# Kernel tuning notes

Hardware: AMD Instinct MI355X
Metric: run time of the kernel (lower is better)

Reference implementation:

```python
import jax, jax.numpy as jnp
import numpy as np

COMMITMENT_COST = 0.25


def setup_inputs() -> dict:
    key = jax.random.key(0)
    k1, k2 = jax.random.split(key)
    z = jax.random.normal(k1, (16, 1024, 256), dtype=jnp.float32)
    embedding = jax.random.normal(k2, (8192, 256), dtype=jnp.float32)
    return {"z": z, "embedding": embedding}


def reference(z, embedding):
    B, N, C = z.shape
    flat = z.reshape(-1, C)  # (B*N, C)
    d = (
        jnp.sum(flat * flat, axis=1, keepdims=True)
        + jnp.sum(embedding * embedding, axis=1)
        - 2.0 * jnp.matmul(flat, embedding.T)
    )  # (B*N, K)
    idx = jnp.argmin(d, axis=1)  # (B*N,)
    quantized = jnp.take(embedding, idx, axis=0).reshape(B, N, C)
    # losses (matching torch detach semantics; in eval fwd-only these are plain MSEs)
    e_latent_loss = jnp.mean((jax.lax.stop_gradient(quantized) - z) ** 2)
    q_latent_loss = jnp.mean((quantized - jax.lax.stop_gradient(z)) ** 2)
    vq_loss = q_latent_loss + COMMITMENT_COST * e_latent_loss
    # straight-through estimator
    quantized_ste = z + jax.lax.stop_gradient(quantized - z)
    encoding_indices = idx.reshape(B, N)
    return quantized_ste, vq_loss, encoding_indices
```

## Files before the change

kernel.cpp:

```cpp
#include <hip/hip_runtime.h>
#include <math.h>

#define MROWS   16384
#define KCODES  8192
#define CDIM    256

#define LOSS_OFF 4194304
#define IDXOFF   4194305

#define NSPLIT  8
#define WS_EF   0
#define WS_ZF   (WS_EF + KCODES * CDIM * 2)
#define WS_EN   (WS_ZF + MROWS * CDIM * 2)
#define WS_PI   (WS_EN + KCODES * 4)
#define WS_PD   (WS_PI + NSPLIT * MROWS * 4)

#define CODES_PER_SPLIT (KCODES / NSPLIT)
#define STEPS32 (CODES_PER_SPLIT / 32)

typedef float    v4f __attribute__((ext_vector_type(4)));
typedef _Float16 v8h __attribute__((ext_vector_type(8)));
typedef __attribute__((address_space(1))) const unsigned int gu32;
typedef __attribute__((address_space(3))) unsigned int su32;

__global__ void conv_kernel(const float* __restrict__ z,
                            const float* __restrict__ emb,
                            char* __restrict__ ws,
                            float* __restrict__ loss_slot) {
    int t = blockIdx.x * 256 + threadIdx.x;
    const int NZ = MROWS * 32;
    const float4* s4;
    _Float16* dst;
    int j, c;
    bool isE = (t >= NZ);
    if (!isE) {
        j = t >> 5; c = t & 31;
        s4 = (const float4*)(z + (size_t)j * CDIM) + c * 2;
        dst = (_Float16*)(ws + WS_ZF);
    } else {
        int u = t - NZ;
        j = u >> 5; c = u & 31;
        s4 = (const float4*)(emb + (size_t)j * CDIM) + c * 2;
        dst = (_Float16*)(ws + WS_EF);
    }
    float4 a = s4[0], b = s4[1];
    v8h h;
    h[0] = (_Float16)a.x; h[1] = (_Float16)a.y;
    h[2] = (_Float16)a.z; h[3] = (_Float16)a.w;
    h[4] = (_Float16)b.x; h[5] = (_Float16)b.y;
    h[6] = (_Float16)b.z; h[7] = (_Float16)b.w;
    *(v8h*)(dst + ((size_t)(j >> 4) * 32 + c) * 128 + (j & 15) * 8) = h;
    if (isE) {
        float s = a.x * a.x + a.y * a.y + a.z * a.z + a.w * a.w +
                  b.x * b.x + b.y * b.y + b.z * b.z + b.w * b.w;
#pragma unroll
        for (int m = 1; m <= 16; m <<= 1) s += __shfl_xor(s, m, 64);
        if (c == 0) ((float*)(ws + WS_EN))[j] = s + 1024.0f;
    }
    if (t == 0) *loss_slot = 0.f;
}

__global__ __launch_bounds__(256, 2)
void vq_pass1_kernel(const char* __restrict__ ws_c, char* __restrict__ ws) {
    __shared__ __attribute__((aligned(16))) char bbuf[2][16384];
    int tid  = threadIdx.x;
    int lane = tid & 63;
    int w    = tid >> 6;
    int tm   = lane & 15;
    int q    = lane >> 4;

    int b  = blockIdx.x;
    int sp = b & 7;
    int rb = b >> 3;
    int r0 = rb * 256 + w * 64;

    const _Float16* zf_g = (const _Float16*)(ws_c + WS_ZF);
    v8h zf[4][8];
#pragma unroll
    for (int mi = 0; mi < 4; ++mi) {
        const _Float16* zr = zf_g + (size_t)((r0 >> 4) + mi) * 4096 + q * 128 + tm * 8;
#pragma unroll
        for (int kc = 0; kc < 8; ++kc)
            zf[mi][kc] = *(const v8h*)(zr + kc * 512);
    }

    const char*  efb  = ws_c + WS_EF + (size_t)(sp * 64) * 8192;
    const float* en_g = (const float*)(ws_c + WS_EN);

#define STAGE(st, bi) do {                                                      \
        const char* g0 = efb + (size_t)(st) * 16384 + w * 4096 + lane * 16;     \
        char* l0 = &bbuf[bi][w * 4096];                                         \
        __builtin_amdgcn_global_load_lds((gu32*)g0, (su32*)l0, 16, 0, 0);       \
        __builtin_amdgcn_global_load_lds((gu32*)(g0 + 1024),                    \
                                         (su32*)(l0 + 1024), 16, 0, 0);         \
        __builtin_amdgcn_global_load_lds((gu32*)(g0 + 2048),                    \
                                         (su32*)(l0 + 2048), 16, 0, 0);         \
        __builtin_amdgcn_global_load_lds((gu32*)(g0 + 3072),                    \
                                         (su32*)(l0 + 3072), 16, 0, 0);         \
    } while (0)

    unsigned rk[16];
#pragma unroll
    for (int s = 0; s < 16; ++s) rk[s] = 0xFFFFFFFFu;

    STAGE(0, 0);
    float enr0 = en_g[sp * 1024 + tm];
    float enr1 = en_g[sp * 1024 + 16 + tm];
    __syncthreads();

#pragma unroll 1
    for (int st = 0; st < STEPS32; ++st) {
        int cur = st & 1;
        if (st < STEPS32 - 1) STAGE(st + 1, cur ^ 1);
        int stn = (st < STEPS32 - 1) ? st + 1 : st;
        float enn0 = en_g[sp * 1024 + stn * 32 + tm];
        float enn1 = en_g[sp * 1024 + stn * 32 + 16 + tm];

#pragma unroll
        for (int ct = 0; ct < 2; ++ct) {
            const char* lb = &bbuf[cur][ct * 8192 + q * 256 + tm * 16];
            v8h bf[8];
#pragma unroll
            for (int kc = 0; kc < 8; ++kc) bf[kc] = *(const v8h*)(lb + kc * 1024);

            v4f acc[4];
#pragma unroll
            for (int mi = 0; mi < 4; ++mi)
                acc[mi] = __builtin_amdgcn_mfma_f32_16x16x32_f16(zf[mi][0], bf[0], (v4f)0.f, 0, 0, 0);
#pragma unroll
            for (int kc = 1; kc < 8; ++kc)
#pragma unroll
                for (int mi = 0; mi < 4; ++mi)
                    acc[mi] = __builtin_amdgcn_mfma_f32_16x16x32_f16(zf[mi][kc], bf[kc], acc[mi], 0, 0, 0);

            float enc = ct ? enr1 : enr0;
            unsigned tag = (unsigned)(st * 2 + ct);
#pragma unroll
            for (int mi = 0; mi < 4; ++mi)
#pragma unroll
                for (int r = 0; r < 4; ++r) {
                    float s = fmaf(-2.f, acc[mi][r], enc);
                    unsigned key = (__float_as_uint(s) << 6) | tag;
                    int slot = mi * 4 + r;
                    rk[slot] = key < rk[slot] ? key : rk[slot];
                }
        }
        enr0 = enn0; enr1 = enn1;
        __syncthreads();
    }
#undef STAGE

#pragma unroll
    for (int slot = 0; slot < 16; ++slot) {
        unsigned k = rk[slot];
        int      t_ = tm;
#pragma unroll
        for (int m = 1; m <= 8; m <<= 1) {
            unsigned k2 = __shfl_xor(k, m, 64);
            int      t2 = __shfl_xor(t_, m, 64);
            if (k2 < k || (k2 == k && t2 < t_)) { k = k2; t_ = t2; }
        }
        if (tm == 0) {
            int row = r0 + (slot >> 2) * 16 + q * 4 + (slot & 3);
            int bi  = sp * 1024 + (int)(k & 63u) * 16 + t_;
            ((int*)(ws + WS_PI))[sp * MROWS + row] = bi;
            ((float*)(ws + WS_PD))[sp * MROWS + row] =
                __uint_as_float((k >> 6) | (17u << 26));
        }
    }
}

__global__ void rerank_out_kernel(const float* __restrict__ z,
                                  const float* __restrict__ emb,
                                  const char* __restrict__ ws,
                                  float* __restrict__ out) {
    __shared__ float wsum[4];
    const int*   pi = (const int*)(ws + WS_PI);
    const float* pd = (const float*)(ws + WS_PD);
    int tid = threadIdx.x, lane = tid & 63, w = tid >> 6;
    int g = lane >> 3, sub = lane & 7;
    const float4* e4 = (const float4*)emb;
    const float4* z4 = (const float4*)z;
    float lsum = 0.f;

#pragma unroll 1
    for (int it = 0; it < 4; ++it) {
        int row = it * 4096 + blockIdx.x * 4 + w;
        int ci   = pi[g * MROWS + row];
        float pg = pd[g * MROWS + row];
        float dmin = pg;
#pragma unroll
        for (int m = 8; m <= 32; m <<= 1) dmin = fminf(dmin, __shfl_xor(dmin, m, 64));
        float s;
        if (pg <= dmin + 0.75f) {
            s = 0.f;
#pragma unroll
            for (int j = 0; j < 8; ++j) {
                float4 ev = e4[(size_t)ci * 64 + sub * 8 + j];
                float4 zv = z4[(size_t)row * 64 + sub * 8 + j];
                float dx = ev.x - zv.x, dy = ev.y - zv.y;
                float dz = ev.z - zv.z, dw = ev.w - zv.w;
                s += dx * dx + dy * dy + dz * dz + dw * dw;
            }
        } else {
            s = 3e38f;
        }
#pragma unroll
        for (int m = 1; m <= 4; m <<= 1) s += __shfl_xor(s, m, 64);
        float dv = s; int di = ci;
#pragma unroll
        for (int m = 8; m <= 32; m <<= 1) {
            float d2 = __shfl_xor(dv, m, 64);
            int   i2 = __shfl_xor(di, m, 64);
            if (d2 < dv || (d2 == dv && i2 < di)) { dv = d2; di = i2; }
        }
        if (lane == 0) out[IDXOFF + row] = (float)di;
        float4 qv = e4[(size_t)di * 64 + lane];
        float4 zv = z4[(size_t)row * 64 + lane];
        float dx = qv.x - zv.x, dy = qv.y - zv.y;
        float dz = qv.z - zv.z, dw = qv.w - zv.w;
        float4 o;
        o.x = zv.x + dx; o.y = zv.y + dy; o.z = zv.z + dz; o.w = zv.w + dw;
        ((float4*)out)[(size_t)row * 64 + lane] = o;
        lsum += dx * dx + dy * dy + dz * dz + dw * dw;
    }

#pragma unroll
    for (int m = 32; m >= 1; m >>= 1) lsum += __shfl_xor(lsum, m, 64);
    if (lane == 0) wsum[w] = lsum;
    __syncthreads();
    if (tid == 0)
        atomicAdd(out + LOSS_OFF,
                  (wsum[0] + wsum[1] + wsum[2] + wsum[3]) * (1.25f / 4194304.f));
}

extern "C" void kernel_launch(void* const* d_in, const int* in_sizes, int n_in,
                              void* d_out, int out_size, void* d_ws, size_t ws_size,
                              hipStream_t stream) {
    const float* z   = (const float*)d_in[0];
    const float* emb = (const float*)d_in[1];
    float* out = (float*)d_out;
    char*  ws  = (char*)d_ws;

    hipLaunchKernelGGL(conv_kernel, dim3((MROWS + KCODES) * 32 / 256), dim3(256),
                       0, stream, z, emb, ws, out + LOSS_OFF);
    hipLaunchKernelGGL(vq_pass1_kernel, dim3((MROWS / 256) * NSPLIT), dim3(256),
                       0, stream, ws, ws);
    hipLaunchKernelGGL(rerank_out_kernel, dim3(1024), dim3(256),
                       0, stream, z, emb, ws, out);
}
```

Baseline: 168.5 us.

## Fuse z fp16 conversion into distance kernel and double code tile per stage

Removes the separate z-to-fp16 conversion pass and its workspace buffer: the distance kernel now loads z in fp32 directly into registers and converts it there, overlapping with the first codebook stage. The LDS double buffer grows to 64 codes per stage, halving the number of barrier-separated iterations, and code norms are now loaded per tile rather than prefetched. This saves a global write and read of z in fp16, but each of the 8 split blocks now rereads fp32 z, and the larger LDS use may reduce occupancy.

Result: slower. 173.6 us (+3.0%).

```diff
diff --git a/kernel.cpp b/kernel.cpp
--- a/kernel.cpp
+++ b/kernel.cpp
@@ -10,59 +10,44 @@
 
 #define NSPLIT  8
 #define WS_EF   0
-#define WS_ZF   (WS_EF + KCODES * CDIM * 2)
-#define WS_EN   (WS_ZF + MROWS * CDIM * 2)
+#define WS_EN   (WS_EF + KCODES * CDIM * 2)
 #define WS_PI   (WS_EN + KCODES * 4)
 #define WS_PD   (WS_PI + NSPLIT * MROWS * 4)
 
 #define CODES_PER_SPLIT (KCODES / NSPLIT)
-#define STEPS32 (CODES_PER_SPLIT / 32)
+#define STEPS64 (CODES_PER_SPLIT / 64)
 
 typedef float    v4f __attribute__((ext_vector_type(4)));
 typedef _Float16 v8h __attribute__((ext_vector_type(8)));
 typedef __attribute__((address_space(1))) const unsigned int gu32;
 typedef __attribute__((address_space(3))) unsigned int su32;
 
-__global__ void conv_kernel(const float* __restrict__ z,
-                            const float* __restrict__ emb,
+__global__ void conv_kernel(const float* __restrict__ emb,
                             char* __restrict__ ws,
                             float* __restrict__ loss_slot) {
     int t = blockIdx.x * 256 + threadIdx.x;
-    const int NZ = MROWS * 32;
-    const float4* s4;
-    _Float16* dst;
-    int j, c;
-    bool isE = (t >= NZ);
-    if (!isE) {
-        j = t >> 5; c = t & 31;
-        s4 = (const float4*)(z + (size_t)j * CDIM) + c * 2;
-        dst = (_Float16*)(ws + WS_ZF);
-    } else {
-        int u = t - NZ;
-        j = u >> 5; c = u & 31;
-        s4 = (const float4*)(emb + (size_t)j * CDIM) + c * 2;
-        dst = (_Float16*)(ws + WS_EF);
-    }
+    int j = t >> 5, c = t & 31;
+    const float4* s4 = (const float4*)(emb + (size_t)j * CDIM) + c * 2;
     float4 a = s4[0], b = s4[1];
     v8h h;
     h[0] = (_Float16)a.x; h[1] = (_Float16)a.y;
     h[2] = (_Float16)a.z; h[3] = (_Float16)a.w;
     h[4] = (_Float16)b.x; h[5] = (_Float16)b.y;
     h[6] = (_Float16)b.z; h[7] = (_Float16)b.w;
-    *(v8h*)(dst + ((size_t)(j >> 4) * 32 + c) * 128 + (j & 15) * 8) = h;
-    if (isE) {
-        float s = a.x * a.x + a.y * a.y + a.z * a.z + a.w * a.w +
-                  b.x * b.x + b.y * b.y + b.z * b.z + b.w * b.w;
-#pragma unroll
-        for (int m = 1; m <= 16; m <<= 1) s += __shfl_xor(s, m, 64);
-        if (c == 0) ((float*)(ws + WS_EN))[j] = s + 1024.0f;
-    }
+    *(v8h*)((_Float16*)(ws + WS_EF) +
+            ((size_t)(j >> 4) * 32 + c) * 128 + (j & 15) * 8) = h;
+    float s = a.x * a.x + a.y * a.y + a.z * a.z + a.w * a.w +
+              b.x * b.x + b.y * b.y + b.z * b.z + b.w * b.w;
+#pragma unroll
+    for (int m = 1; m <= 16; m <<= 1) s += __shfl_xor(s, m, 64);
+    if (c == 0) ((float*)(ws + WS_EN))[j] = s + 1024.0f;
     if (t == 0) *loss_slot = 0.f;
 }
 
 __global__ __launch_bounds__(256, 2)
-void vq_pass1_kernel(const char* __restrict__ ws_c, char* __restrict__ ws) {
-    __shared__ __attribute__((aligned(16))) char bbuf[2][16384];
+void vq_pass1_kernel(const float* __restrict__ z,
+                     const char* __restrict__ ws_c, char* __restrict__ ws) {
+    __shared__ __attribute__((aligned(16))) char bbuf[2][32768];
     int tid  = threadIdx.x;
     int lane = tid & 63;
     int w    = tid >> 6;
@@ -74,22 +59,12 @@
     int rb = b >> 3;
     int r0 = rb * 256 + w * 64;
 
-    const _Float16* zf_g = (const _Float16*)(ws_c + WS_ZF);
-    v8h zf[4][8];
-#pragma unroll
-    for (int mi = 0; mi < 4; ++mi) {
-        const _Float16* zr = zf_g + (size_t)((r0 >> 4) + mi) * 4096 + q * 128 + tm * 8;
-#pragma unroll
-        for (int kc = 0; kc < 8; ++kc)
-            zf[mi][kc] = *(const v8h*)(zr + kc * 512);
-    }
-
     const char*  efb  = ws_c + WS_EF + (size_t)(sp * 64) * 8192;
     const float* en_g = (const float*)(ws_c + WS_EN);
 
 #define STAGE(st, bi) do {                                                      \
-        const char* g0 = efb + (size_t)(st) * 16384 + w * 4096 + lane * 16;     \
-        char* l0 = &bbuf[bi][w * 4096];                                         \
+        const char* g0 = efb + (size_t)(st) * 32768 + w * 8192 + lane * 16;     \
+        char* l0 = &bbuf[bi][w * 8192];                                         \
         __builtin_amdgcn_global_load_lds((gu32*)g0, (su32*)l0, 16, 0, 0);       \
         __builtin_amdgcn_global_load_lds((gu32*)(g0 + 1024),                    \
                                          (su32*)(l0 + 1024), 16, 0, 0);         \
@@ -97,31 +72,53 @@
                                          (su32*)(l0 + 2048), 16, 0, 0);         \
         __builtin_amdgcn_global_load_lds((gu32*)(g0 + 3072),                    \
                                          (su32*)(l0 + 3072), 16, 0, 0);         \
+        __builtin_amdgcn_global_load_lds((gu32*)(g0 + 4096),                    \
+                                         (su32*)(l0 + 4096), 16, 0, 0);         \
+        __builtin_amdgcn_global_load_lds((gu32*)(g0 + 5120),                    \
+                                         (su32*)(l0 + 5120), 16, 0, 0);         \
+        __builtin_amdgcn_global_load_lds((gu32*)(g0 + 6144),                    \
+                                         (su32*)(l0 + 6144), 16, 0, 0);         \
+        __builtin_amdgcn_global_load_lds((gu32*)(g0 + 7168),                    \
+                                         (su32*)(l0 + 7168), 16, 0, 0);         \
     } while (0)
 
+    STAGE(0, 0);
+
+    v8h zf[4][8];
+#pragma unroll
+    for (int mi = 0; mi < 4; ++mi) {
+        const float* zr = z + (size_t)(r0 + mi * 16 + tm) * 256 + q * 8;
+#pragma unroll
+        for (int kc = 0; kc < 8; ++kc) {
+            float4 a = *(const float4*)(zr + kc * 32);
+            float4 bb = *(const float4*)(zr + kc * 32 + 4);
+            v8h h;
+            h[0] = (_Float16)a.x;  h[1] = (_Float16)a.y;
+            h[2] = (_Float16)a.z;  h[3] = (_Float16)a.w;
+            h[4] = (_Float16)bb.x; h[5] = (_Float16)bb.y;
+            h[6] = (_Float16)bb.z; h[7] = (_Float16)bb.w;
+            zf[mi][kc] = h;
+        }
+    }
+
     unsigned rk[16];
 #pragma unroll
     for (int s = 0; s < 16; ++s) rk[s] = 0xFFFFFFFFu;
 
-    STAGE(0, 0);
-    float enr0 = en_g[sp * 1024 + tm];
-    float enr1 = en_g[sp * 1024 + 16 + tm];
     __syncthreads();
 
 #pragma unroll 1
-    for (int st = 0; st < STEPS32; ++st) {
+    for (int st = 0; st < STEPS64; ++st) {
         int cur = st & 1;
-        if (st < STEPS32 - 1) STAGE(st + 1, cur ^ 1);
-        int stn = (st < STEPS32 - 1) ? st + 1 : st;
-        float enn0 = en_g[sp * 1024 + stn * 32 + tm];
-        float enn1 = en_g[sp * 1024 + stn * 32 + 16 + tm];
-
-#pragma unroll
-        for (int ct = 0; ct < 2; ++ct) {
+        if (st < STEPS64 - 1) STAGE(st + 1, cur ^ 1);
+
+#pragma unroll
+        for (int ct = 0; ct < 4; ++ct) {
             const char* lb = &bbuf[cur][ct * 8192 + q * 256 + tm * 16];
             v8h bf[8];
 #pragma unroll
             for (int kc = 0; kc < 8; ++kc) bf[kc] = *(const v8h*)(lb + kc * 1024);
+            float enc = en_g[sp * 1024 + st * 64 + ct * 16 + tm];
 
             v4f acc[4];
 #pragma unroll
@@ -133,8 +130,7 @@
                 for (int mi = 0; mi < 4; ++mi)
                     acc[mi] = __builtin_amdgcn_mfma_f32_16x16x32_f16(zf[mi][kc], bf[kc], acc[mi], 0, 0, 0);
 
-            float enc = ct ? enr1 : enr0;
-            unsigned tag = (unsigned)(st * 2 + ct);
+            unsigned tag = (unsigned)(st * 4 + ct);
 #pragma unroll
             for (int mi = 0; mi < 4; ++mi)
 #pragma unroll
@@ -145,7 +141,6 @@
                     rk[slot] = key < rk[slot] ? key : rk[slot];
                 }
         }
-        enr0 = enn0; enr1 = enn1;
         __syncthreads();
     }
 #undef STAGE
@@ -242,10 +237,10 @@
     float* out = (float*)d_out;
     char*  ws  = (char*)d_ws;
 
-    hipLaunchKernelGGL(conv_kernel, dim3((MROWS + KCODES) * 32 / 256), dim3(256),
-                       0, stream, z, emb, ws, out + LOSS_OFF);
+    hipLaunchKernelGGL(conv_kernel, dim3(KCODES * 32 / 256), dim3(256),
+                       0, stream, emb, ws, out + LOSS_OFF);
     hipLaunchKernelGGL(vq_pass1_kernel, dim3((MROWS / 256) * NSPLIT), dim3(256),
-                       0, stream, ws, ws);
+                       0, stream, z, ws, ws);
     hipLaunchKernelGGL(rerank_out_kernel, dim3(1024), dim3(256),
                        0, stream, z, emb, ws, out);
 }
```
